# Performance work log

Measured on AMD Instinct MI355X. Metric: run time of the kernel, lower is better.

Reference implementation:

```python
import jax, jax.numpy as jnp
import numpy as np
import math

B, H, W = 4, 256, 256
S = 256          # num_superpixels
ZD = 128         # z_dim
GC = 256         # g_channels
NBLK = 8


def setup_inputs() -> dict:
    key = jax.random.key(0)
    ks = jax.random.split(key, 12)
    rn = lambda k, shp, s=1.0: jax.random.normal(k, shp, jnp.float32) * s
    return {
        "z": rn(ks[0], (B, ZD)),
        "images": rn(ks[1], (B, 3, H, W)),
        "segments": jax.random.randint(ks[2], (B, H, W), 0, S).astype(jnp.int32),
        # row-stochastic-ish adjacency scale keeps 8 propagations stable
        "A": rn(ks[3], (B, S, S), 1.0 / math.sqrt(S)),
        # WSConv2d weights: init N(0,1); forward multiplies input by sqrt(2/(in*k*k))
        "proj_w": rn(ks[4], (GC, 3 + ZD)), "proj_b": jnp.zeros((GC,), jnp.float32),
        "blk_proj_w": rn(ks[5], (NBLK, GC, GC)), "blk_proj_b": jnp.zeros((NBLK, GC), jnp.float32),
        "ada1_w": rn(ks[6], (NBLK, 2 * GC, GC)), "ada1_b": jnp.zeros((NBLK, 2 * GC), jnp.float32),
        "ada2_w": rn(ks[7], (NBLK, 2 * GC, 2 * GC)), "ada2_b": jnp.zeros((NBLK, 2 * GC), jnp.float32),
        # plain Conv2d 3x3 layers in upsample head
        "up1_w": rn(ks[8], (GC // 2, GC, 3, 3), 0.02), "up1_b": jnp.zeros((GC // 2,), jnp.float32),
        "up2_w": rn(ks[9], (3, GC // 2, 3, 3), 0.02), "up2_b": jnp.zeros((3,), jnp.float32),
    }


def _ws1x1(x, w, b):
    # WSConv2d with 1x1 kernel over node dim: x [B,Cin,S] -> [B,Cout,S]
    scale = math.sqrt(2.0 / w.shape[1])
    return jnp.einsum('oc,bcs->bos', w, x) * scale + b[None, :, None]


def _conv3(x, w, b):
    y = jax.lax.conv_general_dilated(x, w, (1, 1), 'SAME',
                                     dimension_numbers=('NCHW', 'OIHW', 'NCHW'))
    return y + b[None, :, None, None]


def _forward(z, images, A, proj_w, proj_b, blk_proj_w, blk_proj_b,
             ada1_w, ada1_b, ada2_w, ada2_b, up1_w, up1_b, up2_w, up2_b,
             segments):
    Bn, _, Hn, Wn = images.shape
    N = Hn * Wn
    flat = images.reshape(Bn, 3, N)            # [B,3,N]
    seg = segments.reshape(Bn, N)              # [B,N] int

    # superpixel mean pooling (math of one_hot^T @ flat / counts, as segment-sum)
    seg_sum = jax.vmap(lambda f, s: jax.ops.segment_sum(f, s, num_segments=S))(
        flat.transpose(0, 2, 1), seg)          # [B,S,3]
    counts = jax.vmap(lambda s: jax.ops.segment_sum(
        jnp.ones(s.shape, jnp.float32), s, num_segments=S))(seg)  # [B,S]
    feats = seg_sum / (counts[..., None] + 1e-6)

    z_rep = jnp.broadcast_to(z[:, None, :], (Bn, S, ZD))
    x = jnp.concatenate([feats, z_rep], axis=2).transpose(0, 2, 1)  # [B,3+ZD,S]
    x = _ws1x1(x, proj_w, proj_b)                                   # [B,GC,S]

    for i in range(NBLK):
        h = _ws1x1(x, blk_proj_w[i], blk_proj_b[i])
        # A @ feat : out[b,c,i] = sum_j A[b,i,j] h[b,c,j]
        h = jnp.einsum('bij,bcj->bci', A, h)
        # AdaIN: style from global mean over nodes
        m = h.mean(axis=2, keepdims=True)                    # [B,GC,1]
        s1 = jax.nn.leaky_relu(_ws1x1(m, ada1_w[i], ada1_b[i]), 0.2)
        style = _ws1x1(s1, ada2_w[i], ada2_b[i])             # [B,2GC,1]
        gamma, beta = jnp.split(style, 2, axis=1)
        h = gamma * h + beta
        x = jax.nn.leaky_relu(h, 0.2)                        # dropout=0 (eval)

    # broadcast superpixel feats back to pixels (math of one_hot @ sup_feats)
    sup_feats = x.transpose(0, 2, 1)                         # [B,S,GC]
    pix = jnp.take_along_axis(sup_feats, seg[:, :, None].astype(jnp.int32), axis=1)  # [B,N,GC]
    pix = pix.transpose(0, 2, 1).reshape(Bn, GC, Hn, Wn)

    y = jax.nn.leaky_relu(_conv3(pix, up1_w, up1_b), 0.2)
    y = _conv3(y, up2_w, up2_b)                              # [B,3,H,W]
    # InstanceNorm2d(3), affine=False, eps=1e-5
    mu = y.mean((2, 3), keepdims=True)
    var = y.var((2, 3), keepdims=True)
    y = (y - mu) / jnp.sqrt(var + 1e-5)
    return jnp.tanh(y)


def reference(z, images, segments, A, proj_w, proj_b, blk_proj_w, blk_proj_b,
              ada1_w, ada1_b, ada2_w, ada2_b, up1_w, up1_b, up2_w, up2_b):
    return _forward(z, images, A, proj_w, proj_b, blk_proj_w, blk_proj_b,
                    ada1_w, ada1_b, ada2_w, ada2_b, up1_w, up1_b, up2_w, up2_b,
                    segments)
```

## Files before the change

### kernel.cpp

```cpp
#include <hip/hip_runtime.h>
#include <cmath>

#define BB 4
#define SS 256
#define ZDIM 128
#define GCH 256
#define NBLKS 8
#define NPIX 65536
#define U1C 128

__device__ __forceinline__ float lrelu(float x){ return x >= 0.f ? x : 0.2f*x; }

__global__ __launch_bounds__(256) void k_pp(const float* __restrict__ img,
        const int* __restrict__ seg, float* __restrict__ segsum,
        float* __restrict__ counts, const float* __restrict__ A,
        const float* __restrict__ w1, const float* __restrict__ w2,
        float* __restrict__ At2, float* __restrict__ wT, float* __restrict__ w2t){
  int bid = blockIdx.x;
  int tid = threadIdx.x;
  if(bid < 256){
    __shared__ float ls[SS*4];
    for(int j=tid;j<SS*4;j+=256) ls[j]=0.f;
    __syncthreads();
    int b = bid >> 6;
    int base = bid*1024;
    for(int it=0; it<4; it++){
      int idx = base + it*256 + tid;
      int n = idx & (NPIX-1);
      int s = seg[idx];
      atomicAdd(&ls[s*4+0], img[(b*3+0)*NPIX+n]);
      atomicAdd(&ls[s*4+1], img[(b*3+1)*NPIX+n]);
      atomicAdd(&ls[s*4+2], img[(b*3+2)*NPIX+n]);
      atomicAdd(&ls[s*4+3], 1.0f);
    }
    __syncthreads();
    for(int j=tid;j<SS*4;j+=256){
      int s = j>>2, c = j&3;
      float vv = ls[j];
      if(vv != 0.f){
        if(c<3) atomicAdd(&segsum[(b*SS+s)*3+c], vv);
        else    atomicAdd(&counts[b*SS+s], vv);
      }
    }
  } else if(bid < 512){
    __shared__ float t[32][33];
    int sb = bid - 256;
    int b = sb >> 6;
    int bx = (sb & 7)*32, by = ((sb >> 3) & 7)*32;
    int lx = tid & 31, ly4 = (tid >> 5)*4;
    #pragma unroll
    for(int r=0;r<4;r++)
      t[ly4+r][lx] = A[(b<<16) + ((by+ly4+r)<<8) + bx + lx];
    __syncthreads();
    #pragma unroll
    for(int r=0;r<4;r++){
      int jj = bx + ly4 + r;
      int i  = by + lx;
      At2[(b<<16) + ((jj>>2)<<10) + (i<<2) + (jj&3)] = t[lx][ly4+r];
    }
  } else {
    int idx = (bid-512)*256 + tid;
    if(idx < 294912){
      int o = idx & 127; int r = idx >> 7; int c = r & 255; int k = r >> 8;
      wT[idx] = w1[(o*GCH + c)*9 + k];
    } else if(idx < 294912 + 3456){
      int t2 = idx - 294912;
      int cc = t2 & 7;
      int oc = (t2 >> 3) % 3;
      int sg = (t2 / 24) & 3;
      int g  = (t2 / 96) & 3;
      int k  = t2 / 384;
      w2t[t2] = w2[oc*1152 + (g*32 + sg*8 + cc)*9 + k];
    }
  }
}

__global__ __launch_bounds__(256) void k_x0(const float* __restrict__ segsum,
        const float* __restrict__ counts, const float* __restrict__ z,
        const float* __restrict__ pw, const float* __restrict__ pb,
        float sc, float4* __restrict__ xp2){
  int og = blockIdx.x;
  int b  = blockIdx.y;
  int i  = threadIdx.x;
  float cnt = counts[b*SS+i] + 1e-6f;
  float f0 = segsum[(b*SS+i)*3+0]/cnt;
  float f1 = segsum[(b*SS+i)*3+1]/cnt;
  float f2 = segsum[(b*SS+i)*3+2]/cnt;
  const float* zb = z + b*ZDIM;
  float vals[4];
  #pragma unroll
  for(int oo=0;oo<4;oo++){
    int o = og*4 + oo;
    const float* wr = pw + o*131;
    float acc = wr[0]*f0 + wr[1]*f1 + wr[2]*f2;
    #pragma unroll 8
    for(int j=0;j<ZDIM;j++) acc += wr[3+j]*zb[j];
    vals[oo] = acc*sc + pb[o];
  }
  float4 o4 = {vals[0], vals[1], vals[2], vals[3]};
  xp2[(b*64+og)*256 + i] = o4;
}

__global__ __launch_bounds__(512) void k_gemm(const float4* __restrict__ xp2,
        const float* __restrict__ bw, const float* __restrict__ bb,
        const float4* __restrict__ At2, float sc,
        float* __restrict__ h2, float* __restrict__ m){
  int c0 = blockIdx.x*4;
  int b  = blockIdx.y;
  int tid = threadIdx.x;
  int j  = tid & 255;
  int h  = tid >> 8;
  __shared__ float4 wl4[4][64];
  __shared__ float ps[8][260];
  __shared__ float4 h1l4[4][66];
  __shared__ float red[4][4];
  for(int t = tid; t < 1024; t += 512){
    int row = t >> 8, jj = t & 255;
    ((float*)&wl4[row][0])[jj] = bw[(c0+row)*GCH + jj];
  }
  __syncthreads();
  {
    const float4* xb = xp2 + (b*64 + h*32)*256 + j;
    float a0=0.f, a1=0.f, a2=0.f, a3=0.f;
    #pragma unroll 8
    for(int kg=0; kg<32; kg++){
      float4 x  = xb[kg*256];
      float4 w0 = wl4[0][h*32+kg];
      float4 w1v= wl4[1][h*32+kg];
      float4 w2v= wl4[2][h*32+kg];
      float4 w3 = wl4[3][h*32+kg];
      a0 += w0.x*x.x + w0.y*x.y + w0.z*x.z + w0.w*x.w;
      a1 += w1v.x*x.x + w1v.y*x.y + w1v.z*x.z + w1v.w*x.w;
      a2 += w2v.x*x.x + w2v.y*x.y + w2v.z*x.z + w2v.w*x.w;
      a3 += w3.x*x.x + w3.y*x.y + w3.z*x.z + w3.w*x.w;
    }
    ps[0+h][j] = a0; ps[2+h][j] = a1; ps[4+h][j] = a2; ps[6+h][j] = a3;
  }
  __syncthreads();
  if(tid < 256){
    #pragma unroll
    for(int ch=0;ch<4;ch++){
      float vv = (ps[ch*2][tid] + ps[ch*2+1][tid])*sc + bb[c0+ch];
      ((float*)&h1l4[ch][0])[tid] = vv;
    }
  }
  __syncthreads();
  {
    const float4* ab = At2 + (b*64 + h*32)*256 + j;
    float r0=0.f, r1=0.f, r2=0.f, r3=0.f;
    #pragma unroll 8
    for(int kg=0; kg<32; kg++){
      float4 a  = ab[kg*256];
      float4 h0 = h1l4[0][h*32+kg];
      float4 h1 = h1l4[1][h*32+kg];
      float4 h2v= h1l4[2][h*32+kg];
      float4 h3 = h1l4[3][h*32+kg];
      r0 += a.x*h0.x + a.y*h0.y + a.z*h0.z + a.w*h0.w;
      r1 += a.x*h1.x + a.y*h1.y + a.z*h1.z + a.w*h1.w;
      r2 += a.x*h2v.x + a.y*h2v.y + a.z*h2v.z + a.w*h2v.w;
      r3 += a.x*h3.x + a.y*h3.y + a.z*h3.z + a.w*h3.w;
    }
    ps[0+h][j] = r0; ps[2+h][j] = r1; ps[4+h][j] = r2; ps[6+h][j] = r3;
  }
  __syncthreads();
  float rr0=0.f, rr1=0.f, rr2=0.f, rr3=0.f;
  if(tid < 256){
    rr0 = ps[0][tid]+ps[1][tid];
    rr1 = ps[2][tid]+ps[3][tid];
    rr2 = ps[4][tid]+ps[5][tid];
    rr3 = ps[6][tid]+ps[7][tid];
    h2[(b*GCH+c0+0)*SS + tid] = rr0;
    h2[(b*GCH+c0+1)*SS + tid] = rr1;
    h2[(b*GCH+c0+2)*SS + tid] = rr2;
    h2[(b*GCH+c0+3)*SS + tid] = rr3;
  }
  for(int off=32; off; off>>=1){
    rr0 += __shfl_down(rr0,off); rr1 += __shfl_down(rr1,off);
    rr2 += __shfl_down(rr2,off); rr3 += __shfl_down(rr3,off);
  }
  if(tid < 256 && (tid & 63)==0){
    int w3 = tid >> 6;
    red[0][w3]=rr0; red[1][w3]=rr1; red[2][w3]=rr2; red[3][w3]=rr3;
  }
  __syncthreads();
  if(tid < 4)
    m[b*GCH + c0 + tid] =
      (red[tid][0]+red[tid][1]+red[tid][2]+red[tid][3])*(1.f/256.f);
}

__global__ __launch_bounds__(512) void k_s12(const float* __restrict__ m,
        const float* __restrict__ a1w, const float* __restrict__ a1b,
        const float* __restrict__ a2w, const float* __restrict__ a2b,
        const float* __restrict__ h2, float sc1, float sc2,
        float4* __restrict__ xp2){
  int q = blockIdx.x;
  int tid = threadIdx.x;
  int lane = tid & 63, wv = tid >> 6;
  int grp = lane >> 3, ll = lane & 7;
  __shared__ float4 ml4[256];
  __shared__ float s1l[4][512];
  __shared__ float gbl[4][16];
  if(tid < 256) ml4[tid] = ((const float4*)m)[tid];
  __syncthreads();
  #pragma unroll 2
  for(int pass=0; pass<8; pass++){
    int row = wv*64 + pass*8 + grp;
    const float4* ar = (const float4*)(a1w + row*GCH) + ll;
    float p0=0.f,p1=0.f,p2=0.f,p3=0.f;
    #pragma unroll
    for(int j=0;j<8;j++){
      float4 w4 = ar[j*8];
      float4 m0 = ml4[0*64 + j*8 + ll];
      float4 m1 = ml4[1*64 + j*8 + ll];
      float4 m2 = ml4[2*64 + j*8 + ll];
      float4 m3 = ml4[3*64 + j*8 + ll];
      p0 += w4.x*m0.x + w4.y*m0.y + w4.z*m0.z + w4.w*m0.w;
      p1 += w4.x*m1.x + w4.y*m1.y + w4.z*m1.z + w4.w*m1.w;
      p2 += w4.x*m2.x + w4.y*m2.y + w4.z*m2.z + w4.w*m2.w;
      p3 += w4.x*m3.x + w4.y*m3.y + w4.z*m3.z + w4.w*m3.w;
    }
    #pragma unroll
    for(int off=1; off<8; off<<=1){
      p0 += __shfl_xor(p0,off); p1 += __shfl_xor(p1,off);
      p2 += __shfl_xor(p2,off); p3 += __shfl_xor(p3,off);
    }
    if(ll == 0){
      float bv = a1b[row];
      int sidx = ((row & 7) << 6) + (row >> 3);
      s1l[0][sidx] = lrelu(p0*sc1 + bv);
      s1l[1][sidx] = lrelu(p1*sc1 + bv);
      s1l[2][sidx] = lrelu(p2*sc1 + bv);
      s1l[3][sidx] = lrelu(p3*sc1 + bv);
    }
  }
  __syncthreads();
  float sA[4][8];
  #pragma unroll
  for(int b=0;b<4;b++)
    #pragma unroll
    for(int j=0;j<8;j++) sA[b][j] = s1l[b][j*64 + lane];
  #pragma unroll
  for(int r=0;r<2;r++){
    int ridx = wv*2 + r;
    int cc = ridx & 7;
    int t = (ridx < 8) ? (q*8 + cc) : (256 + q*8 + cc);
    const float* wr = a2w + t*512 + lane*8;
    float4 wa = *(const float4*)wr;
    float4 wb4 = *(const float4*)(wr+4);
    float p0 = wa.x*sA[0][0]+wa.y*sA[0][1]+wa.z*sA[0][2]+wa.w*sA[0][3]
             + wb4.x*sA[0][4]+wb4.y*sA[0][5]+wb4.z*sA[0][6]+wb4.w*sA[0][7];
    float p1 = wa.x*sA[1][0]+wa.y*sA[1][1]+wa.z*sA[1][2]+wa.w*sA[1][3]
             + wb4.x*sA[1][4]+wb4.y*sA[1][5]+wb4.z*sA[1][6]+wb4.w*sA[1][7];
    float p2 = wa.x*sA[2][0]+wa.y*sA[2][1]+wa.z*sA[2][2]+wa.w*sA[2][3]
             + wb4.x*sA[2][4]+wb4.y*sA[2][5]+wb4.z*sA[2][6]+wb4.w*sA[2][7];
    float p3 = wa.x*sA[3][0]+wa.y*sA[3][1]+wa.z*sA[3][2]+wa.w*sA[3][3]
             + wb4.x*sA[3][4]+wb4.y*sA[3][5]+wb4.z*sA[3][6]+wb4.w*sA[3][7];
    for(int off=32; off; off>>=1){
      p0 += __shfl_xor(p0,off); p1 += __shfl_xor(p1,off);
      p2 += __shfl_xor(p2,off); p3 += __shfl_xor(p3,off);
    }
    if(lane < 4){
      float p = lane==0 ? p0 : lane==1 ? p1 : lane==2 ? p2 : p3;
      gbl[lane][ridx] = p*sc2 + a2b[t];
    }
  }
  __syncthreads();
  int j = tid & 255;
  int cg2 = tid >> 8;
  int cbase = q*8 + cg2*4;
  int cg = cbase >> 2;
  #pragma unroll
  for(int b=0;b<4;b++){
    float4 o;
    o.x = lrelu(gbl[b][cg2*4+0]*h2[(b*GCH + cbase+0)*SS + j] + gbl[b][8+cg2*4+0]);
    o.y = lrelu(gbl[b][cg2*4+1]*h2[(b*GCH + cbase+1)*SS + j] + gbl[b][8+cg2*4+1]);
    o.z = lrelu(gbl[b][cg2*4+2]*h2[(b*GCH + cbase+2)*SS + j] + gbl[b][8+cg2*4+2]);
    o.w = lrelu(gbl[b][cg2*4+3]*h2[(b*GCH + cbase+3)*SS + j] + gbl[b][8+cg2*4+3]);
    xp2[(b*64 + cg)*256 + j] = o;
  }
}

__global__ __launch_bounds__(256) void k_v(const float4* __restrict__ xp2,
        const float4* __restrict__ wT4, float4* __restrict__ v4){
  int s0 = blockIdx.x*16;
  int k  = blockIdx.y;
  int b  = blockIdx.z;
  int tid = threadIdx.x;
  __shared__ float4 wl[64][33];
  __shared__ float xft[256][17];
  for(int t = tid; t < 1024; t += 256){
    int cg = t >> 4, si = t & 15;
    float4 xv = xp2[(b*64 + cg)*256 + s0 + si];
    xft[cg*4+0][si] = xv.x;
    xft[cg*4+1][si] = xv.y;
    xft[cg*4+2][si] = xv.z;
    xft[cg*4+3][si] = xv.w;
  }
  int og = tid & 31, sh = tid >> 5;
  const float4* wb = wT4 + (size_t)k*GCH*32;
  float4 a0 = {0.f,0.f,0.f,0.f}, a1 = {0.f,0.f,0.f,0.f};
  for(int ct=0; ct<4; ct++){
    __syncthreads();
    for(int t = tid; t < 2048; t += 256){
      int cc = t>>5, o = t&31;
      wl[cc][o] = wb[(ct*64+cc)*32 + o];
    }
    __syncthreads();
    #pragma unroll 4
    for(int cc=0;cc<64;cc++){
      float4 w = wl[cc][og];
      int c = ct*64+cc;
      float x0v = xft[c][sh];
      float x1v = xft[c][8+sh];
      a0.x += w.x*x0v; a0.y += w.y*x0v; a0.z += w.z*x0v; a0.w += w.w*x0v;
      a1.x += w.x*x1v; a1.y += w.y*x1v; a1.z += w.z*x1v; a1.w += w.w*x1v;
    }
  }
  size_t base = (size_t)(b*9+k)*SS + s0;
  v4[(base + sh)*32 + og]     = a0;
  v4[(base + 8 + sh)*32 + og] = a1;
}

__global__ __launch_bounds__(256) void k_conv(const float4* __restrict__ v4,
        const int* __restrict__ seg, const float4* __restrict__ b14,
        const float* __restrict__ w2t, float* __restrict__ y2){
  __shared__ float4 y1t4[100*9];
  __shared__ int   segl[144];
  __shared__ float part[768];
  int bid = blockIdx.x;
  int x = bid & 7;
  int b = x >> 1;
  int sub = ((bid >> 3) << 1) + (x & 1);
  int g = sub & 3;
  int tile = sub >> 2;
  int x0p = (tile & 31)*8, y0p = (tile >> 5)*8;
  int tid = threadIdx.x;
  if(tid < 144){
    int r = tid/12, cc = tid%12;
    int gy = y0p - 2 + r, gx = x0p - 2 + cc;
    segl[tid] = (gy>=0 && gy<256 && gx>=0 && gx<256) ? seg[(b*256+gy)*256+gx] : -1;
  }
  __syncthreads();
  int o2 = tid & 3;
  const float4* vb = v4 + (size_t)(b*9)*SS*32 + g*8 + o2*2;
  float4 biasA = b14[g*8 + o2*2];
  float4 biasB = b14[g*8 + o2*2 + 1];
  bool interior = (x0p >= 8 && x0p <= 240 && y0p >= 8 && y0p <= 240);
  if(interior){
    for(int task = tid; task < 400; task += 256){
      int pp = task >> 2;
      int py = pp/10, px = pp - py*10;
      float4 aA = biasA, aB = biasB;
      #pragma unroll
      for(int k=0;k<9;k++){
        int sidx = segl[(py + k/3)*12 + (px + k%3)];
        const float4* pv = vb + (k*SS + sidx)*32;
        float4 vA = pv[0], vB = pv[1];
        aA.x += vA.x; aA.y += vA.y; aA.z += vA.z; aA.w += vA.w;
        aB.x += vB.x; aB.y += vB.y; aB.z += vB.z; aB.w += vB.w;
      }
      float4 valA, valB;
      valA.x = lrelu(aA.x); valA.y = lrelu(aA.y); valA.z = lrelu(aA.z); valA.w = lrelu(aA.w);
      valB.x = lrelu(aB.x); valB.y = lrelu(aB.y); valB.z = lrelu(aB.z); valB.w = lrelu(aB.w);
      y1t4[pp*9 + o2*2]     = valA;
      y1t4[pp*9 + o2*2 + 1] = valB;
    }
  } else {
    for(int task = tid; task < 400; task += 256){
      int pp = task >> 2;
      int py = pp/10, px = pp - py*10;
      int gy = y0p - 1 + py, gx = x0p - 1 + px;
      bool pix_ok = (gy>=0 && gy<256 && gx>=0 && gx<256);
      float4 aA = biasA, aB = biasB;
      #pragma unroll
      for(int k=0;k<9;k++){
        int sidx = segl[(py + k/3)*12 + (px + k%3)];
        int sidx0 = sidx < 0 ? 0 : sidx;
        float msk = sidx < 0 ? 0.f : 1.f;
        const float4* pv = vb + (k*SS + sidx0)*32;
        float4 vA = pv[0], vB = pv[1];
        aA.x += msk*vA.x; aA.y += msk*vA.y; aA.z += msk*vA.z; aA.w += msk*vA.w;
        aB.x += msk*vB.x; aB.y += msk*vB.y; aB.z += msk*vB.z; aB.w += msk*vB.w;
      }
      float4 valA, valB;
      valA.x = pix_ok ? lrelu(aA.x) : 0.f;
      valA.y = pix_ok ? lrelu(aA.y) : 0.f;
      valA.z = pix_ok ? lrelu(aA.z) : 0.f;
      valA.w = pix_ok ? lrelu(aA.w) : 0.f;
      valB.x = pix_ok ? lrelu(aB.x) : 0.f;
      valB.y = pix_ok ? lrelu(aB.y) : 0.f;
      valB.z = pix_ok ? lrelu(aB.z) : 0.f;
      valB.w = pix_ok ? lrelu(aB.w) : 0.f;
      y1t4[pp*9 + o2*2]     = valA;
      y1t4[pp*9 + o2*2 + 1] = valB;
    }
  }
  __syncthreads();
  int pxo = tid & 63, sg = tid >> 6;
  int sgu = __builtin_amdgcn_readfirstlane(sg);
  const float* wk0 = w2t + (g*4 + sgu)*24;
  int ty = pxo >> 3, tx = pxo & 7;
  float p0=0.f,p1=0.f,p2=0.f;
  #pragma unroll
  for(int k=0;k<9;k++){
    int pp0 = (ty + k/3)*10 + (tx + k%3);
    float4 ya = y1t4[pp0*9 + sgu*2];
    float4 yb = y1t4[pp0*9 + sgu*2 + 1];
    const float* wk = wk0 + k*384;
    p0 += wk[0]*ya.x + wk[1]*ya.y + wk[2]*ya.z + wk[3]*ya.w
        + wk[4]*yb.x + wk[5]*yb.y + wk[6]*yb.z + wk[7]*yb.w;
    p1 += wk[8]*ya.x + wk[9]*ya.y + wk[10]*ya.z + wk[11]*ya.w
        + wk[12]*yb.x + wk[13]*yb.y + wk[14]*yb.z + wk[15]*yb.w;
    p2 += wk[16]*ya.x + wk[17]*ya.y + wk[18]*ya.z + wk[19]*ya.w
        + wk[20]*yb.x + wk[21]*yb.y + wk[22]*yb.z + wk[23]*yb.w;
  }
  part[tid]     = p0;
  part[256+tid] = p1;
  part[512+tid] = p2;
  __syncthreads();
  if(tid < 64){
    float s0 = part[tid]    +part[tid+64]    +part[tid+128]    +part[tid+192];
    float s1 = part[256+tid]+part[256+tid+64]+part[256+tid+128]+part[256+tid+192];
    float s2 = part[512+tid]+part[512+tid+64]+part[512+tid+128]+part[512+tid+192];
    int gy = y0p + (tid>>3), gx = x0p + (tid&7);
    int nidx = gy*256+gx;
    atomicAdd(&y2[(b*3+0)*NPIX+nidx], s0);
    atomicAdd(&y2[(b*3+1)*NPIX+nidx], s1);
    atomicAdd(&y2[(b*3+2)*NPIX+nidx], s2);
  }
}

__global__ void k_stats(const float* __restrict__ y2, double* __restrict__ stats){
  int bc = blockIdx.x;
  int chunk = blockIdx.y;
  const float* p = y2 + (size_t)bc*NPIX + chunk*8192;
  int t = threadIdx.x;
  double s=0.0, q=0.0;
  for(int i=t;i<8192;i+=256){ double vv = (double)p[i]; s+=vv; q+=vv*vv; }
  __shared__ double rs[256], rq[256];
  rs[t]=s; rq[t]=q; __syncthreads();
  for(int st=128; st; st>>=1){ if(t<st){rs[t]+=rs[t+st]; rq[t]+=rq[t+st];} __syncthreads(); }
  if(t==0){ atomicAdd(&stats[bc*2], rs[0]); atomicAdd(&stats[bc*2+1], rq[0]); }
}

__global__ void k_norm(const float* __restrict__ y2, const double* __restrict__ stats,
                       float* __restrict__ out){
  int bu = (blockIdx.x*256) >> 16;
  double mu  = stats[bu*2+0] * (1.0/65536.0);
  double ex2 = stats[bu*2+1] * (1.0/65536.0);
  double var = ex2 - mu*mu;
  float inv = (float)(1.0/sqrt(var + 1e-5));
  float mf = (float)mu;
  int idx = blockIdx.x*256+threadIdx.x;
  out[idx] = tanhf((y2[idx]-mf)*inv);
}

extern "C" void kernel_launch(void* const* d_in, const int* in_sizes, int n_in,
                              void* d_out, int out_size, void* d_ws, size_t ws_size,
                              hipStream_t stream) {
  const float* z   = (const float*)d_in[0];
  const float* img = (const float*)d_in[1];
  const int*   seg = (const int*)d_in[2];
  const float* A   = (const float*)d_in[3];
  const float* pw  = (const float*)d_in[4];
  const float* pb  = (const float*)d_in[5];
  const float* bw  = (const float*)d_in[6];
  const float* bb  = (const float*)d_in[7];
  const float* a1w = (const float*)d_in[8];
  const float* a1b = (const float*)d_in[9];
  const float* a2w = (const float*)d_in[10];
  const float* a2b = (const float*)d_in[11];
  const float* w1  = (const float*)d_in[12];
  const float* b1  = (const float*)d_in[13];
  const float* w2  = (const float*)d_in[14];
  const float* b2  = (const float*)d_in[15]; (void)b2;
  float* out = (float*)d_out;

  float* ws = (float*)d_ws;
  float* segsum = ws;
  float* counts = ws + 3072;
  float* m      = ws + 4096;
  double* stats = (double*)(ws + 5120);
  float* xp2 = ws + 5248;
  float* h2  = xp2 + 262144;
  float* At2 = h2 + 262144;
  float* wT  = At2 + 262144;
  float* v   = wT + 294912;
  float* y2  = v + 1179648;
  float* w2t = y2 + 786432;

  hipMemsetAsync(ws, 0, 5248*sizeof(float), stream);
  hipMemsetAsync(y2, 0, 786432*sizeof(float), stream);

  float sProj = (float)sqrt(2.0/131.0);
  float s256  = (float)sqrt(2.0/256.0);
  float s512  = (float)sqrt(2.0/512.0);

  k_pp  <<<512 + 1166, 256, 0, stream>>>(img, seg, segsum, counts,
                                         A, w1, w2, At2, wT, w2t);
  k_x0  <<<dim3(64,4), 256, 0, stream>>>(segsum, counts, z, pw, pb, sProj,
                                         (float4*)xp2);

  for(int blk=0; blk<NBLKS; blk++){
    k_gemm<<<dim3(64,4), 512, 0, stream>>>((const float4*)xp2,
                                           bw + blk*GCH*GCH, bb + blk*GCH,
                                           (const float4*)At2, s256, h2, m);
    k_s12 <<<32, 512, 0, stream>>>(m, a1w + blk*512*GCH, a1b + blk*512,
                                   a2w + blk*512*512, a2b + blk*512,
                                   h2, s256, s512, (float4*)xp2);
  }

  k_v   <<<dim3(16,9,4), 256, 0, stream>>>((const float4*)xp2, (const float4*)wT,
                                           (float4*)v);
  k_conv<<<16384, 256, 0, stream>>>((const float4*)v, seg, (const float4*)b1, w2t, y2);
  k_stats<<<dim3(12,8), 256, 0, stream>>>(y2, stats);
  k_norm<<<3072, 256, 0, stream>>>(y2, stats, out);
}
```

Baseline: 371.3 us.

## Fuse GNN block kernels using column-mean of A to compute style in parallel

Merges the per-block gemm and style kernels into one launch. The node-mean of A·(W·x) is computed algebraically from the column means of A, which are precomputed once, so the style MLP can run in separate workgroups alongside the propagation GEMM instead of waiting for it. The style affine and leaky-relu of the previous block are applied lazily when the next kernel reads its input, and ping-pong buffers carry the state between blocks. This halves the kernel launches per block and removes a serial dependency. In exchange the style workgroups recompute the previous block's activations and the reassociated sums change floating-point rounding.

```diff
diff --git a/kernel.cpp b/kernel.cpp
--- a/kernel.cpp
+++ b/kernel.cpp
@@ -15,7 +15,8 @@
         const int* __restrict__ seg, float* __restrict__ segsum,
         float* __restrict__ counts, const float* __restrict__ A,
         const float* __restrict__ w1, const float* __restrict__ w2,
-        float* __restrict__ At2, float* __restrict__ wT, float* __restrict__ w2t){
+        float* __restrict__ At2, float* __restrict__ Am,
+        float* __restrict__ wT, float* __restrict__ w2t){
   int bid = blockIdx.x;
   int tid = threadIdx.x;
   if(bid < 256){
@@ -58,8 +59,19 @@
       int i  = by + lx;
       At2[(b<<16) + ((jj>>2)<<10) + (i<<2) + (jj&3)] = t[lx][ly4+r];
     }
+  } else if(bid < 516){
+    int b = bid - 512;
+    int j = tid;
+    float s0=0.f,s1=0.f,s2=0.f,s3=0.f;
+    for(int i=0;i<256;i+=4){
+      s0 += A[(b<<16)+((i+0)<<8)+j];
+      s1 += A[(b<<16)+((i+1)<<8)+j];
+      s2 += A[(b<<16)+((i+2)<<8)+j];
+      s3 += A[(b<<16)+((i+3)<<8)+j];
+    }
+    Am[b*256+j] = ((s0+s1)+(s2+s3))*(1.f/256.f);
   } else {
-    int idx = (bid-512)*256 + tid;
+    int idx = (bid-516)*256 + tid;
     if(idx < 294912){
       int o = idx & 127; int r = idx >> 7; int c = r & 255; int k = r >> 8;
       wT[idx] = w1[(o*GCH + c)*9 + k];
@@ -101,200 +113,215 @@
   xp2[(b*64+og)*256 + i] = o4;
 }
 
-__global__ __launch_bounds__(512) void k_gemm(const float4* __restrict__ xp2,
-        const float* __restrict__ bw, const float* __restrict__ bb,
-        const float4* __restrict__ At2, float sc,
-        float* __restrict__ h2, float* __restrict__ m){
-  int c0 = blockIdx.x*4;
-  int b  = blockIdx.y;
-  int tid = threadIdx.x;
-  int j  = tid & 255;
-  int h  = tid >> 8;
-  __shared__ float4 wl4[4][64];
-  __shared__ float ps[8][260];
-  __shared__ float4 h1l4[4][66];
-  __shared__ float red[4][4];
-  for(int t = tid; t < 1024; t += 512){
-    int row = t >> 8, jj = t & 255;
-    ((float*)&wl4[row][0])[jj] = bw[(c0+row)*GCH + jj];
-  }
-  __syncthreads();
-  {
-    const float4* xb = xp2 + (b*64 + h*32)*256 + j;
-    float a0=0.f, a1=0.f, a2=0.f, a3=0.f;
-    #pragma unroll 8
-    for(int kg=0; kg<32; kg++){
-      float4 x  = xb[kg*256];
-      float4 w0 = wl4[0][h*32+kg];
-      float4 w1v= wl4[1][h*32+kg];
-      float4 w2v= wl4[2][h*32+kg];
-      float4 w3 = wl4[3][h*32+kg];
-      a0 += w0.x*x.x + w0.y*x.y + w0.z*x.z + w0.w*x.w;
-      a1 += w1v.x*x.x + w1v.y*x.y + w1v.z*x.z + w1v.w*x.w;
-      a2 += w2v.x*x.x + w2v.y*x.y + w2v.z*x.z + w2v.w*x.w;
-      a3 += w3.x*x.x + w3.y*x.y + w3.z*x.z + w3.w*x.w;
-    }
-    ps[0+h][j] = a0; ps[2+h][j] = a1; ps[4+h][j] = a2; ps[6+h][j] = a3;
-  }
-  __syncthreads();
-  if(tid < 256){
-    #pragma unroll
-    for(int ch=0;ch<4;ch++){
-      float vv = (ps[ch*2][tid] + ps[ch*2+1][tid])*sc + bb[c0+ch];
-      ((float*)&h1l4[ch][0])[tid] = vv;
-    }
-  }
-  __syncthreads();
-  {
-    const float4* ab = At2 + (b*64 + h*32)*256 + j;
-    float r0=0.f, r1=0.f, r2=0.f, r3=0.f;
-    #pragma unroll 8
-    for(int kg=0; kg<32; kg++){
-      float4 a  = ab[kg*256];
-      float4 h0 = h1l4[0][h*32+kg];
-      float4 h1 = h1l4[1][h*32+kg];
-      float4 h2v= h1l4[2][h*32+kg];
-      float4 h3 = h1l4[3][h*32+kg];
-      r0 += a.x*h0.x + a.y*h0.y + a.z*h0.z + a.w*h0.w;
-      r1 += a.x*h1.x + a.y*h1.y + a.z*h1.z + a.w*h1.w;
-      r2 += a.x*h2v.x + a.y*h2v.y + a.z*h2v.z + a.w*h2v.w;
-      r3 += a.x*h3.x + a.y*h3.y + a.z*h3.z + a.w*h3.w;
-    }
-    ps[0+h][j] = r0; ps[2+h][j] = r1; ps[4+h][j] = r2; ps[6+h][j] = r3;
-  }
-  __syncthreads();
-  float rr0=0.f, rr1=0.f, rr2=0.f, rr3=0.f;
-  if(tid < 256){
-    rr0 = ps[0][tid]+ps[1][tid];
-    rr1 = ps[2][tid]+ps[3][tid];
-    rr2 = ps[4][tid]+ps[5][tid];
-    rr3 = ps[6][tid]+ps[7][tid];
-    h2[(b*GCH+c0+0)*SS + tid] = rr0;
-    h2[(b*GCH+c0+1)*SS + tid] = rr1;
-    h2[(b*GCH+c0+2)*SS + tid] = rr2;
-    h2[(b*GCH+c0+3)*SS + tid] = rr3;
-  }
-  for(int off=32; off; off>>=1){
-    rr0 += __shfl_down(rr0,off); rr1 += __shfl_down(rr1,off);
-    rr2 += __shfl_down(rr2,off); rr3 += __shfl_down(rr3,off);
-  }
-  if(tid < 256 && (tid & 63)==0){
-    int w3 = tid >> 6;
-    red[0][w3]=rr0; red[1][w3]=rr1; red[2][w3]=rr2; red[3][w3]=rr3;
-  }
-  __syncthreads();
-  if(tid < 4)
-    m[b*GCH + c0 + tid] =
-      (red[tid][0]+red[tid][1]+red[tid][2]+red[tid][3])*(1.f/256.f);
-}
-
-__global__ __launch_bounds__(512) void k_s12(const float* __restrict__ m,
-        const float* __restrict__ a1w, const float* __restrict__ a1b,
-        const float* __restrict__ a2w, const float* __restrict__ a2b,
-        const float* __restrict__ h2, float sc1, float sc2,
-        float4* __restrict__ xp2){
-  int q = blockIdx.x;
+__global__ __launch_bounds__(512) void k_iter(
+    const float4* __restrict__ h2prev, const float* __restrict__ gbPrev,
+    float4* __restrict__ h2next, float* __restrict__ gbNext,
+    const float* __restrict__ bw, const float* __restrict__ bb,
+    const float* __restrict__ a1w, const float* __restrict__ a1b,
+    const float* __restrict__ a2w, const float* __restrict__ a2b,
+    const float4* __restrict__ At2, const float* __restrict__ Am,
+    float sc, float sc2){
+  int bid = blockIdx.x;
   int tid = threadIdx.x;
   int lane = tid & 63, wv = tid >> 6;
-  int grp = lane >> 3, ll = lane & 7;
-  __shared__ float4 ml4[256];
-  __shared__ float s1l[4][512];
-  __shared__ float gbl[4][16];
-  if(tid < 256) ml4[tid] = ((const float4*)m)[tid];
-  __syncthreads();
-  #pragma unroll 2
-  for(int pass=0; pass<8; pass++){
-    int row = wv*64 + pass*8 + grp;
-    const float4* ar = (const float4*)(a1w + row*GCH) + ll;
-    float p0=0.f,p1=0.f,p2=0.f,p3=0.f;
+  if(bid < 32){
+    __shared__ float amL[256];
+    __shared__ float4 glS4[128];
+    __shared__ float4 xm4[64];
+    __shared__ float4 mL4[64];
+    __shared__ float4 s1L4[128];
+    int b = bid & 3, q = bid >> 2;
+    if(tid < 256) amL[tid] = Am[b*256 + tid];
+    if(gbPrev) ((float*)glS4)[tid] = gbPrev[b*512 + tid];
+    __syncthreads();
+    float sp = amL[lane] + amL[lane+64] + amL[lane+128] + amL[lane+192];
     #pragma unroll
-    for(int j=0;j<8;j++){
-      float4 w4 = ar[j*8];
-      float4 m0 = ml4[0*64 + j*8 + ll];
-      float4 m1 = ml4[1*64 + j*8 + ll];
-      float4 m2 = ml4[2*64 + j*8 + ll];
-      float4 m3 = ml4[3*64 + j*8 + ll];
-      p0 += w4.x*m0.x + w4.y*m0.y + w4.z*m0.z + w4.w*m0.w;
-      p1 += w4.x*m1.x + w4.y*m1.y + w4.z*m1.z + w4.w*m1.w;
-      p2 += w4.x*m2.x + w4.y*m2.y + w4.z*m2.z + w4.w*m2.w;
-      p3 += w4.x*m3.x + w4.y*m3.y + w4.z*m3.z + w4.w*m3.w;
-    }
+    for(int off=32; off; off>>=1) sp += __shfl_xor(sp, off);
+    float SAm = sp;
+    const float4* hp = h2prev + (size_t)(b*64)*256;
     #pragma unroll
-    for(int off=1; off<8; off<<=1){
-      p0 += __shfl_xor(p0,off); p1 += __shfl_xor(p1,off);
-      p2 += __shfl_xor(p2,off); p3 += __shfl_xor(p3,off);
-    }
-    if(ll == 0){
-      float bv = a1b[row];
-      int sidx = ((row & 7) << 6) + (row >> 3);
-      s1l[0][sidx] = lrelu(p0*sc1 + bv);
-      s1l[1][sidx] = lrelu(p1*sc1 + bv);
-      s1l[2][sidx] = lrelu(p2*sc1 + bv);
-      s1l[3][sidx] = lrelu(p3*sc1 + bv);
-    }
-  }
-  __syncthreads();
-  float sA[4][8];
-  #pragma unroll
-  for(int b=0;b<4;b++)
-    #pragma unroll
-    for(int j=0;j<8;j++) sA[b][j] = s1l[b][j*64 + lane];
-  #pragma unroll
-  for(int r=0;r<2;r++){
-    int ridx = wv*2 + r;
-    int cc = ridx & 7;
-    int t = (ridx < 8) ? (q*8 + cc) : (256 + q*8 + cc);
-    const float* wr = a2w + t*512 + lane*8;
-    float4 wa = *(const float4*)wr;
-    float4 wb4 = *(const float4*)(wr+4);
-    float p0 = wa.x*sA[0][0]+wa.y*sA[0][1]+wa.z*sA[0][2]+wa.w*sA[0][3]
-             + wb4.x*sA[0][4]+wb4.y*sA[0][5]+wb4.z*sA[0][6]+wb4.w*sA[0][7];
-    float p1 = wa.x*sA[1][0]+wa.y*sA[1][1]+wa.z*sA[1][2]+wa.w*sA[1][3]
-             + wb4.x*sA[1][4]+wb4.y*sA[1][5]+wb4.z*sA[1][6]+wb4.w*sA[1][7];
-    float p2 = wa.x*sA[2][0]+wa.y*sA[2][1]+wa.z*sA[2][2]+wa.w*sA[2][3]
-             + wb4.x*sA[2][4]+wb4.y*sA[2][5]+wb4.z*sA[2][6]+wb4.w*sA[2][7];
-    float p3 = wa.x*sA[3][0]+wa.y*sA[3][1]+wa.z*sA[3][2]+wa.w*sA[3][3]
-             + wb4.x*sA[3][4]+wb4.y*sA[3][5]+wb4.z*sA[3][6]+wb4.w*sA[3][7];
-    for(int off=32; off; off>>=1){
-      p0 += __shfl_xor(p0,off); p1 += __shfl_xor(p1,off);
-      p2 += __shfl_xor(p2,off); p3 += __shfl_xor(p3,off);
-    }
-    if(lane < 4){
-      float p = lane==0 ? p0 : lane==1 ? p1 : lane==2 ? p2 : p3;
-      gbl[lane][ridx] = p*sc2 + a2b[t];
-    }
-  }
-  __syncthreads();
-  int j = tid & 255;
-  int cg2 = tid >> 8;
-  int cbase = q*8 + cg2*4;
-  int cg = cbase >> 2;
-  #pragma unroll
-  for(int b=0;b<4;b++){
-    float4 o;
-    o.x = lrelu(gbl[b][cg2*4+0]*h2[(b*GCH + cbase+0)*SS + j] + gbl[b][8+cg2*4+0]);
-    o.y = lrelu(gbl[b][cg2*4+1]*h2[(b*GCH + cbase+1)*SS + j] + gbl[b][8+cg2*4+1]);
-    o.z = lrelu(gbl[b][cg2*4+2]*h2[(b*GCH + cbase+2)*SS + j] + gbl[b][8+cg2*4+2]);
-    o.w = lrelu(gbl[b][cg2*4+3]*h2[(b*GCH + cbase+3)*SS + j] + gbl[b][8+cg2*4+3]);
-    xp2[(b*64 + cg)*256 + j] = o;
-  }
-}
-
-__global__ __launch_bounds__(256) void k_v(const float4* __restrict__ xp2,
+    for(int p=0;p<8;p++){
+      int kg = wv*8 + p;
+      float4 acc = {0.f,0.f,0.f,0.f};
+      if(gbPrev){
+        float4 g4 = glS4[kg];
+        float4 t4 = glS4[64 + kg];
+        #pragma unroll
+        for(int jj=0;jj<4;jj++){
+          int j = jj*64 + lane;
+          float4 h = hp[kg*256 + j];
+          float a = amL[j];
+          acc.x += a*lrelu(g4.x*h.x + t4.x);
+          acc.y += a*lrelu(g4.y*h.y + t4.y);
+          acc.z += a*lrelu(g4.z*h.z + t4.z);
+          acc.w += a*lrelu(g4.w*h.w + t4.w);
+        }
+      } else {
+        #pragma unroll
+        for(int jj=0;jj<4;jj++){
+          int j = jj*64 + lane;
+          float4 h = hp[kg*256 + j];
+          float a = amL[j];
+          acc.x += a*h.x; acc.y += a*h.y; acc.z += a*h.z; acc.w += a*h.w;
+        }
+      }
+      #pragma unroll
+      for(int off=32; off; off>>=1){
+        acc.x += __shfl_xor(acc.x,off); acc.y += __shfl_xor(acc.y,off);
+        acc.z += __shfl_xor(acc.z,off); acc.w += __shfl_xor(acc.w,off);
+      }
+      if(lane==0) xm4[kg] = acc;
+    }
+    __syncthreads();
+    float4 xmv = xm4[lane];
+    for(int r=0;r<32;r++){
+      int c = wv*32 + r;
+      float4 w4 = ((const float4*)(bw + c*GCH))[lane];
+      float pd = w4.x*xmv.x + w4.y*xmv.y + w4.z*xmv.z + w4.w*xmv.w;
+      #pragma unroll
+      for(int off=32; off; off>>=1) pd += __shfl_xor(pd,off);
+      if(lane==0) ((float*)mL4)[c] = sc*pd + bb[c]*SAm;
+    }
+    __syncthreads();
+    float4 mv = mL4[lane];
+    for(int r=0;r<64;r++){
+      int row = wv*64 + r;
+      float4 w4 = ((const float4*)(a1w + row*GCH))[lane];
+      float pd = w4.x*mv.x + w4.y*mv.y + w4.z*mv.z + w4.w*mv.w;
+      #pragma unroll
+      for(int off=32; off; off>>=1) pd += __shfl_xor(pd,off);
+      if(lane==0) ((float*)s1L4)[row] = lrelu(sc*pd + a1b[row]);
+    }
+    __syncthreads();
+    float4 sa = s1L4[lane*2];
+    float4 sb = s1L4[lane*2+1];
+    for(int r=0;r<8;r++){
+      int lr = wv*8 + r;
+      int t = (lr < 32) ? (q*32 + lr) : (256 + q*32 + (lr-32));
+      const float4* ar = (const float4*)(a2w + t*512);
+      float4 wa = ar[lane*2], wb4 = ar[lane*2+1];
+      float pd = wa.x*sa.x+wa.y*sa.y+wa.z*sa.z+wa.w*sa.w
+               + wb4.x*sb.x+wb4.y*sb.y+wb4.z*sb.z+wb4.w*sb.w;
+      #pragma unroll
+      for(int off=32; off; off>>=1) pd += __shfl_xor(pd,off);
+      if(lane==0) gbNext[b*512 + t] = sc2*pd + a2b[t];
+    }
+  } else {
+    __shared__ float4 wl4[4][64];
+    __shared__ float4 glG4[128];
+    __shared__ float ps[8][260];
+    __shared__ float4 h1l4[4][66];
+    int idx = bid - 32;
+    int c0 = (idx >> 2)*4;
+    int b  = idx & 3;
+    int j  = tid & 255;
+    int h  = tid >> 8;
+    for(int t = tid; t < 1024; t += 512){
+      int row = t >> 8, jj = t & 255;
+      ((float*)&wl4[row][0])[jj] = bw[(c0+row)*GCH + jj];
+    }
+    if(gbPrev) ((float*)glG4)[tid] = gbPrev[b*512 + tid];
+    __syncthreads();
+    {
+      const float4* xb = h2prev + (size_t)(b*64 + h*32)*256 + j;
+      float a0=0.f, a1=0.f, a2=0.f, a3=0.f;
+      if(gbPrev){
+        #pragma unroll 8
+        for(int kg=0; kg<32; kg++){
+          float4 x = xb[kg*256];
+          int kga = h*32 + kg;
+          float4 g4 = glG4[kga];
+          float4 t4 = glG4[64 + kga];
+          x.x = lrelu(g4.x*x.x + t4.x);
+          x.y = lrelu(g4.y*x.y + t4.y);
+          x.z = lrelu(g4.z*x.z + t4.z);
+          x.w = lrelu(g4.w*x.w + t4.w);
+          float4 w0 = wl4[0][kga];
+          float4 w1v= wl4[1][kga];
+          float4 w2v= wl4[2][kga];
+          float4 w3 = wl4[3][kga];
+          a0 += w0.x*x.x + w0.y*x.y + w0.z*x.z + w0.w*x.w;
+          a1 += w1v.x*x.x + w1v.y*x.y + w1v.z*x.z + w1v.w*x.w;
+          a2 += w2v.x*x.x + w2v.y*x.y + w2v.z*x.z + w2v.w*x.w;
+          a3 += w3.x*x.x + w3.y*x.y + w3.z*x.z + w3.w*x.w;
+        }
+      } else {
+        #pragma unroll 8
+        for(int kg=0; kg<32; kg++){
+          float4 x = xb[kg*256];
+          int kga = h*32 + kg;
+          float4 w0 = wl4[0][kga];
+          float4 w1v= wl4[1][kga];
+          float4 w2v= wl4[2][kga];
+          float4 w3 = wl4[3][kga];
+          a0 += w0.x*x.x + w0.y*x.y + w0.z*x.z + w0.w*x.w;
+          a1 += w1v.x*x.x + w1v.y*x.y + w1v.z*x.z + w1v.w*x.w;
+          a2 += w2v.x*x.x + w2v.y*x.y + w2v.z*x.z + w2v.w*x.w;
+          a3 += w3.x*x.x + w3.y*x.y + w3.z*x.z + w3.w*x.w;
+        }
+      }
+      ps[0+h][j] = a0; ps[2+h][j] = a1; ps[4+h][j] = a2; ps[6+h][j] = a3;
+    }
+    __syncthreads();
+    if(tid < 256){
+      #pragma unroll
+      for(int ch=0;ch<4;ch++){
+        float vv = (ps[ch*2][tid] + ps[ch*2+1][tid])*sc + bb[c0+ch];
+        ((float*)&h1l4[ch][0])[tid] = vv;
+      }
+    }
+    __syncthreads();
+    {
+      const float4* ab = At2 + (size_t)(b*64 + h*32)*256 + j;
+      float r0=0.f, r1=0.f, r2=0.f, r3=0.f;
+      #pragma unroll 8
+      for(int kg=0; kg<32; kg++){
+        float4 a  = ab[kg*256];
+        float4 h0 = h1l4[0][h*32+kg];
+        float4 h1 = h1l4[1][h*32+kg];
+        float4 h2v= h1l4[2][h*32+kg];
+        float4 h3 = h1l4[3][h*32+kg];
+        r0 += a.x*h0.x + a.y*h0.y + a.z*h0.z + a.w*h0.w;
+        r1 += a.x*h1.x + a.y*h1.y + a.z*h1.z + a.w*h1.w;
+        r2 += a.x*h2v.x + a.y*h2v.y + a.z*h2v.z + a.w*h2v.w;
+        r3 += a.x*h3.x + a.y*h3.y + a.z*h3.z + a.w*h3.w;
+      }
+      ps[0+h][j] = r0; ps[2+h][j] = r1; ps[4+h][j] = r2; ps[6+h][j] = r3;
+    }
+    __syncthreads();
+    if(tid < 256){
+      float4 o;
+      o.x = ps[0][tid]+ps[1][tid];
+      o.y = ps[2][tid]+ps[3][tid];
+      o.z = ps[4][tid]+ps[5][tid];
+      o.w = ps[6][tid]+ps[7][tid];
+      h2next[(size_t)(b*64 + (c0>>2))*256 + tid] = o;
+    }
+  }
+}
+
+__global__ __launch_bounds__(256) void k_v(const float4* __restrict__ h2f,
+        const float* __restrict__ gbF,
         const float4* __restrict__ wT4, float4* __restrict__ v4){
   int s0 = blockIdx.x*16;
   int k  = blockIdx.y;
   int b  = blockIdx.z;
   int tid = threadIdx.x;
+  __shared__ float4 glV4[128];
   __shared__ float4 wl[64][33];
   __shared__ float xft[256][17];
+  ((float*)glV4)[tid] = gbF[b*512 + tid];
+  ((float*)glV4)[256+tid] = gbF[b*512 + 256 + tid];
+  __syncthreads();
   for(int t = tid; t < 1024; t += 256){
     int cg = t >> 4, si = t & 15;
-    float4 xv = xp2[(b*64 + cg)*256 + s0 + si];
-    xft[cg*4+0][si] = xv.x;
-    xft[cg*4+1][si] = xv.y;
-    xft[cg*4+2][si] = xv.z;
-    xft[cg*4+3][si] = xv.w;
+    float4 xv = h2f[(size_t)(b*64 + cg)*256 + s0 + si];
+    float4 g4 = glV4[cg];
+    float4 t4 = glV4[64 + cg];
+    xft[cg*4+0][si] = lrelu(g4.x*xv.x + t4.x);
+    xft[cg*4+1][si] = lrelu(g4.y*xv.y + t4.y);
+    xft[cg*4+2][si] = lrelu(g4.z*xv.z + t4.z);
+    xft[cg*4+3][si] = lrelu(g4.w*xv.w + t4.w);
   }
   int og = tid & 31, sh = tid >> 5;
   const float4* wb = wT4 + (size_t)k*GCH*32;
@@ -479,11 +506,13 @@
   float* ws = (float*)d_ws;
   float* segsum = ws;
   float* counts = ws + 3072;
-  float* m      = ws + 4096;
+  float* Am     = ws + 4096;
   double* stats = (double*)(ws + 5120);
-  float* xp2 = ws + 5248;
-  float* h2  = xp2 + 262144;
-  float* At2 = h2 + 262144;
+  float* gb0 = ws + 5248;
+  float* gb1 = gb0 + 2048;
+  float* h2a = ws + 9344;
+  float* h2b = h2a + 262144;
+  float* At2 = h2b + 262144;
   float* wT  = At2 + 262144;
   float* v   = wT + 294912;
   float* y2  = v + 1179648;
@@ -496,22 +525,27 @@
   float s256  = (float)sqrt(2.0/256.0);
   float s512  = (float)sqrt(2.0/512.0);
 
-  k_pp  <<<512 + 1166, 256, 0, stream>>>(img, seg, segsum, counts,
-                                         A, w1, w2, At2, wT, w2t);
+  k_pp  <<<516 + 1166, 256, 0, stream>>>(img, seg, segsum, counts,
+                                         A, w1, w2, At2, Am, wT, w2t);
   k_x0  <<<dim3(64,4), 256, 0, stream>>>(segsum, counts, z, pw, pb, sProj,
-                                         (float4*)xp2);
+                                         (float4*)h2a);
 
   for(int blk=0; blk<NBLKS; blk++){
-    k_gemm<<<dim3(64,4), 512, 0, stream>>>((const float4*)xp2,
-                                           bw + blk*GCH*GCH, bb + blk*GCH,
-                                           (const float4*)At2, s256, h2, m);
-    k_s12 <<<32, 512, 0, stream>>>(m, a1w + blk*512*GCH, a1b + blk*512,
-                                   a2w + blk*512*512, a2b + blk*512,
-                                   h2, s256, s512, (float4*)xp2);
-  }
-
-  k_v   <<<dim3(16,9,4), 256, 0, stream>>>((const float4*)xp2, (const float4*)wT,
-                                           (float4*)v);
+    const float* h2p = (blk & 1) ? h2b : h2a;
+    float*       h2n = (blk & 1) ? h2a : h2b;
+    const float* gbp = (blk == 0) ? (const float*)nullptr
+                                  : ((blk & 1) ? gb0 : gb1);
+    float*       gbn = (blk & 1) ? gb1 : gb0;
+    k_iter<<<288, 512, 0, stream>>>((const float4*)h2p, gbp,
+                                    (float4*)h2n, gbn,
+                                    bw + blk*GCH*GCH, bb + blk*GCH,
+                                    a1w + blk*512*GCH, a1b + blk*512,
+                                    a2w + blk*512*512, a2b + blk*512,
+                                    (const float4*)At2, Am, s256, s512);
+  }
+
+  k_v   <<<dim3(16,9,4), 256, 0, stream>>>((const float4*)h2a, gb1,
+                                           (const float4*)wT, (float4*)v);
   k_conv<<<16384, 256, 0, stream>>>((const float4*)v, seg, (const float4*)b1, w2t, y2);
   k_stats<<<dim3(12,8), 256, 0, stream>>>(y2, stats);
   k_norm<<<3072, 256, 0, stream>>>(y2, stats, out);
```

After: 684.3 us. +84.3%, slower.
